# Kernel tuning notes

Measured on AMD Instinct MI355X. Metric: run time of the kernel, lower is better.

The kernel has to match this reference:

```python
import jax, jax.numpy as jnp
import numpy as np

WS = (17, 5, 1)
NT = 23  # 17+5+1 tokens across levels
TABLE_ROWS = (2 * WS[0] - 1) * (2 * WS[0] - 1)  # 1089


def _rel_index():
    cs = []
    for i, w in enumerate(WS):
        c = np.arange(w, dtype=np.float32) - w // 2
        if i < len(WS) - 1:
            c = c * WS[0] / w  # rescale coarser levels to finest grid
        cs.append(c)
    c = np.concatenate(cs)  # [23]
    return (c[:, None] - c[None, :]) + (WS[0] - 1)  # [23,23] float

REL_IDX = jnp.asarray(_rel_index())


def _avgpool1d(x):
    # AvgPool1d(kernel=2, stride=2, padding=1, count_include_pad=False) on last axis (odd L)
    return jnp.concatenate([x[..., :1], (x[..., 1::2] + x[..., 2::2]) * 0.5], axis=-1)


def _l2norm(x):
    n = jnp.linalg.norm(x, axis=-1, keepdims=True)
    return x / jnp.maximum(n, 1e-12)


def _pos_embed(table, abs_bias):
    # table [1089,H], abs_bias [3,H,1,1,1] -> [1,H,1,23,23]
    idx = REL_IDX.reshape(-1)
    fl = jnp.clip(jnp.floor(idx), 0, TABLE_ROWS - 1).astype(jnp.int32)
    ce = jnp.clip(jnp.ceil(idx), 0, TABLE_ROWS - 1).astype(jnp.int32)
    w_ce = (idx - fl.astype(idx.dtype))[:, None]
    pe = (1.0 - w_ce) * table[fl] + w_ce * table[ce]  # [529,H]
    H = table.shape[1]
    pe = pe.reshape(1, 1, NT, NT, H).transpose(0, 4, 1, 2, 3)  # [1,H,1,23,23]
    chunks = jnp.split(pe, [WS[0], WS[0] + WS[1]], axis=3)
    chunks = [c + abs_bias[i][None] for i, c in enumerate(chunks)]
    return jnp.concatenate(chunks, axis=-2)


def _hifi(xh0, xh1, xh2, h_table, h_abs, h_proj_w, h_proj_b):
    q = jnp.concatenate([xh0[0], xh1[0], xh2[0]], axis=-2)  # [B,Hh,hd,23,S]
    k = jnp.concatenate([xh0[1], xh1[1], xh2[1]], axis=-2)
    v = jnp.concatenate([xh0[2], xh1[2], xh2[2]], axis=-2)
    attn = jnp.einsum('bhdts,bhdus->bhdtu', _l2norm(q), _l2norm(k))
    attn = attn + _pos_embed(h_table, h_abs)
    attn = jax.nn.softmax(attn, axis=-1)
    out = jnp.einsum('bhdtu,bhdus->bhdts', attn, v)
    return out @ h_proj_w.T + h_proj_b


def _lofi(xl0, xl1, xl2, l_table, l_abs, l_proj_w, l_proj_b):
    q = jnp.concatenate([xl0[0], xl1[0], xl2[0]], axis=-2)  # [B,Hl,hd,23,S]
    kvs = []
    for i, x in enumerate((xl0, xl1, xl2)):
        kv = x[1:]  # [2,B,Hl,hd,t_i,S]
        if i != 2:  # pool token axis for the two finer levels
            kv = jnp.moveaxis(_avgpool1d(jnp.moveaxis(kv, -2, -1)), -1, -2)
        kvs.append(kv)
    kv = jnp.concatenate(kvs, axis=-2)  # [2,B,Hl,hd,13,S]
    k, v = kv[0], kv[1]
    attn = jnp.einsum('bhdts,bhdus->bhdtu', _l2norm(q), _l2norm(k))  # [B,Hl,hd,23,13]
    pe = _pos_embed(l_table, l_abs)  # [1,Hl,1,23,23]
    Hl = l_table.shape[1]
    p1 = _avgpool1d(pe[..., :WS[0]].reshape(Hl, NT, WS[0])).reshape(1, Hl, 1, NT, -1)
    p2 = _avgpool1d(pe[..., WS[0]:WS[0] + WS[1]].reshape(Hl, NT, WS[1])).reshape(1, Hl, 1, NT, -1)
    p3 = pe[..., -1:]
    attn = attn + jnp.concatenate([p1, p2, p3], axis=-1)
    attn = jax.nn.softmax(attn, axis=-1)
    out = jnp.einsum('bhdtu,bhdus->bhdts', attn, v)
    return out @ l_proj_w.T + l_proj_b


def _forward(xh0, xh1, xh2, xl0, xl1, xl2, h_table, h_abs, l_table, l_abs,
             h_proj_w, h_proj_b, l_proj_w, l_proj_b):
    h_out = _hifi(xh0, xh1, xh2, h_table, h_abs, h_proj_w, h_proj_b)  # [B,1,64,23,S]
    l_out = _lofi(xl0, xl1, xl2, l_table, l_abs, l_proj_w, l_proj_b)  # [B,3,64,23,S]
    return jnp.concatenate([h_out, l_out], axis=1)  # [B,4,64,23,S]


def setup_inputs() -> dict:
    key = jax.random.key(0)
    ks = jax.random.split(key, 14)
    B, hd, S = 4, 64, 1024
    Hh, Hl = 1, 3
    d = {
        'xh0': jax.random.normal(ks[0], (3, B, Hh, hd, 17, S), jnp.float32),
        'xh1': jax.random.normal(ks[1], (3, B, Hh, hd, 5, S), jnp.float32),
        'xh2': jax.random.normal(ks[2], (3, B, Hh, hd, 1, S), jnp.float32),
        'xl0': jax.random.normal(ks[3], (3, B, Hl, hd, 17, S), jnp.float32),
        'xl1': jax.random.normal(ks[4], (3, B, Hl, hd, 5, S), jnp.float32),
        'xl2': jax.random.normal(ks[5], (3, B, Hl, hd, 1, S), jnp.float32),
        'h_table': jax.random.normal(ks[6], (TABLE_ROWS, Hh), jnp.float32) * 0.02,
        'h_abs': jax.random.normal(ks[7], (3, Hh, 1, 1, 1), jnp.float32) * 0.02,
        'l_table': jax.random.normal(ks[8], (TABLE_ROWS, Hl), jnp.float32) * 0.02,
        'l_abs': jax.random.normal(ks[9], (3, Hl, 1, 1, 1), jnp.float32) * 0.02,
        'h_proj_w': jax.random.normal(ks[10], (S, S), jnp.float32) / np.sqrt(S),
        'h_proj_b': jax.random.normal(ks[11], (S,), jnp.float32) * 0.01,
        'l_proj_w': jax.random.normal(ks[12], (S, S), jnp.float32) / np.sqrt(S),
        'l_proj_b': jax.random.normal(ks[13], (S,), jnp.float32) * 0.01,
    }
    return d


def reference(xh0, xh1, xh2, xl0, xl1, xl2, h_table, h_abs, l_table, l_abs,
              h_proj_w, h_proj_b, l_proj_w, l_proj_b):
    return _forward(xh0, xh1, xh2, xl0, xl1, xl2, h_table, h_abs, l_table, l_abs,
                    h_proj_w, h_proj_b, l_proj_w, l_proj_b)
```

## Files before the change

kernel.cpp:

```cpp
#include <hip/hip_runtime.h>
#include <hip/hip_bf16.h>
#include <stdint.h>

#define DEV __device__ __forceinline__

typedef float f32x4 __attribute__((ext_vector_type(4)));
typedef __bf16 bf16x8 __attribute__((ext_vector_type(8)));

DEV __bf16 tobf(float x){
  union { __hip_bfloat16 s; __bf16 b; } u; u.s = __float2bfloat16(x); return u.b;
}
DEV float bflo(uint32_t u){ return __uint_as_float(u << 16); }
DEV float bfhi(uint32_t u){ return __uint_as_float(u & 0xffff0000u); }
DEV float dot4(const float4& a, const float4& b){
  return a.x*b.x + a.y*b.y + a.z*b.z + a.w*b.w;
}
DEV bf16x8 pack8(const float4& a, const float4& b){
  bf16x8 r;
  r[0]=tobf(a.x); r[1]=tobf(a.y); r[2]=tobf(a.z); r[3]=tobf(a.w);
  r[4]=tobf(b.x); r[5]=tobf(b.y); r[6]=tobf(b.z); r[7]=tobf(b.w);
  return r;
}
DEV uint32_t f2bf2(float x, float y){
  union { __hip_bfloat16 b[2]; uint32_t u; } cv;
  cv.b[0] = __float2bfloat16(x); cv.b[1] = __float2bfloat16(y);
  return cv.u;
}
DEV float4 avg4(const float4& a, const float4& b){
  float4 r; r.x=0.5f*(a.x+b.x); r.y=0.5f*(a.y+b.y); r.z=0.5f*(a.z+b.z); r.w=0.5f*(a.w+b.w);
  return r;
}

DEV float relc(int j){
  if (j < 17) return (float)(j - 8);
  if (j < 22) return (float)(j - 19) * 3.4f;
  return 0.0f;
}
DEV int band_of(int t){ return t < 17 ? 0 : (t < 22 ? 1 : 2); }

template<int MODE> DEV void pool_map(int u, int& a, int& b){
  if (MODE == 0){ a = u; b = u; return; }
  if (u == 0){ a = 0; b = 0; }
  else if (u < 9){ a = 2*u - 1; b = 2*u; }
  else if (u == 9){ a = 17; b = 17; }
  else if (u < 12){ a = 2*u - 2; b = 2*u - 1; }
  else { a = 22; b = 22; }
}

DEV float interp_tab(const float* tab, int H, int h, int t, int u){
  float idx = relc(t) - relc(u) + 16.0f;
  float fl = floorf(idx);
  float ce = ceilf(idx);
  int fi = (int)fminf(fmaxf(fl, 0.f), 1088.f);
  int ci = (int)fminf(fmaxf(ce, 0.f), 1088.f);
  float w = idx - fl;
  return (1.0f - w) * tab[fi*H + h] + w * tab[ci*H + h];
}

template<int MODE>
DEV void qk_group(int gm, int qt,
    const float* __restrict__ x0, const float* __restrict__ x1, const float* __restrict__ x2,
    float* __restrict__ SpB,
    float* Spart , float* qnp , float* knp )
{
  constexpr int U = (MODE == 0) ? 23 : 13;
  constexpr int H = (MODE == 0) ? 1 : 3;
  int b, h, d;
  if (MODE == 0){ b = gm >> 6; h = 0; d = gm & 63; }
  else { b = gm / 192; int r = gm % 192; h = r >> 6; d = r & 63; }

  const int tid  = threadIdx.x;
  const int lane = tid & 63;
  const int w    = tid >> 6;
  const int lrow = lane & 15;
  const int kq   = lane >> 4;

  auto base_of = [&](int sel, int band) -> const float* {
    if (band == 0) return x0 + (size_t)((((sel*4 + b)*H + h)*64 + d)*17) * 1024;
    if (band == 1) return x1 + (size_t)((((sel*4 + b)*H + h)*64 + d)*5) * 1024;
    return x2 + (size_t)(((sel*4 + b)*H + h)*64 + d) * 1024;
  };
  const float* qb0 = base_of(0,0); const float* qb1 = base_of(0,1); const float* qb2 = base_of(0,2);
  const float* kb0 = base_of(1,0); const float* kb1 = base_of(1,1); const float* kb2 = base_of(1,2);

  auto rowp = [&](const float* r0, const float* r1, const float* r2, int t) -> const float* {
    if (t < 17) return r0 + (size_t)t * 1024;
    if (t < 22) return r1 + (size_t)(t - 17) * 1024;
    return r2;
  };

  const float* qr[2]; bool qv[2];
  #pragma unroll
  for (int mi = 0; mi < 2; ++mi){
    int t = mi*16 + lrow;
    qv[mi] = (t < 23);
    qr[mi] = qv[mi] ? rowp(qb0,qb1,qb2,t) : qb0;
  }
  const float* krA[2]; const float* krB[2]; bool kv[2];
  #pragma unroll
  for (int ni = 0; ni < 2; ++ni){
    int u = ni*16 + lrow;
    kv[ni] = (u < U);
    int au, bu; pool_map<MODE>(kv[ni] ? u : 0, au, bu);
    krA[ni] = rowp(kb0,kb1,kb2,au);
    krB[ni] = rowp(kb0,kb1,kb2,bu);
  }

  const int sbase = qt*256 + w*64 + kq*8;

  float4 qld[2][4];
  float4 kld[2][4];
  #pragma unroll
  for (int mi = 0; mi < 2; ++mi){
    #pragma unroll
    for (int kk = 0; kk < 2; ++kk){
      #pragma unroll
      for (int hf = 0; hf < 2; ++hf){
        qld[mi][kk*2+hf] = qv[mi] ? *(const float4*)(qr[mi] + sbase + kk*32 + hf*4)
                                  : float4{0,0,0,0};
      }
    }
  }
  if (MODE == 0){
    #pragma unroll
    for (int ni = 0; ni < 2; ++ni){
      #pragma unroll
      for (int kk = 0; kk < 2; ++kk){
        #pragma unroll
        for (int hf = 0; hf < 2; ++hf){
          kld[ni][kk*2+hf] = kv[ni] ? *(const float4*)(krA[ni] + sbase + kk*32 + hf*4)
                                    : float4{0,0,0,0};
        }
      }
    }
  } else {
    #pragma unroll
    for (int kk = 0; kk < 2; ++kk){
      #pragma unroll
      for (int hf = 0; hf < 2; ++hf){
        kld[0][kk*2+hf] = kv[0] ? *(const float4*)(krA[0] + sbase + kk*32 + hf*4)
                                : float4{0,0,0,0};
        kld[1][kk*2+hf] = kv[0] ? *(const float4*)(krB[0] + sbase + kk*32 + hf*4)
                                : float4{0,0,0,0};
      }
    }
  }

  f32x4 acc[2][2] = {};
  float qss[2] = {0.f, 0.f}, kss[2] = {0.f, 0.f};
  #pragma unroll
  for (int kk = 0; kk < 2; ++kk){
    bf16x8 qf[2], kf[2];
    #pragma unroll
    for (int mi = 0; mi < 2; ++mi){
      float4 v0 = qld[mi][kk*2], v1 = qld[mi][kk*2+1];
      qss[mi] += dot4(v0,v0) + dot4(v1,v1);
      qf[mi] = pack8(v0, v1);
    }
    if (MODE == 0){
      #pragma unroll
      for (int ni = 0; ni < 2; ++ni){
        float4 v0 = kld[ni][kk*2], v1 = kld[ni][kk*2+1];
        kss[ni] += dot4(v0,v0) + dot4(v1,v1);
        kf[ni] = pack8(v0, v1);
      }
    } else {
      float4 v0 = avg4(kld[0][kk*2], kld[1][kk*2]);
      float4 v1 = avg4(kld[0][kk*2+1], kld[1][kk*2+1]);
      kss[0] += dot4(v0,v0) + dot4(v1,v1);
      kf[0] = pack8(v0, v1);
    }
    #pragma unroll
    for (int mi = 0; mi < 2; ++mi){
      #pragma unroll
      for (int ni = 0; ni < 2; ++ni){
        if (MODE == 0 || ni == 0)
          acc[mi][ni] = __builtin_amdgcn_mfma_f32_16x16x32_bf16(qf[mi], kf[ni], acc[mi][ni], 0, 0, 0);
      }
    }
  }

  #pragma unroll
  for (int i = 0; i < 2; ++i){
    qss[i] += __shfl_xor(qss[i], 16); qss[i] += __shfl_xor(qss[i], 32);
    kss[i] += __shfl_xor(kss[i], 16); kss[i] += __shfl_xor(kss[i], 32);
  }
  if (lane < 16){
    qnp[w*32 + lane]      = qss[0];
    qnp[w*32 + 16 + lane] = qss[1];
    knp[w*32 + lane]      = kss[0];
    knp[w*32 + 16 + lane] = kss[1];
  }
  #pragma unroll
  for (int mi = 0; mi < 2; ++mi)
    #pragma unroll
    for (int ni = 0; ni < 2; ++ni)
      #pragma unroll
      for (int j = 0; j < 4; ++j)
        Spart[w*1056 + (mi*16 + kq*4 + j)*33 + ni*16 + lrow] = acc[mi][ni][j];
  __syncthreads();

  if (tid < 32){
    SpB[1024 + tid] = qnp[tid] + qnp[32+tid] + qnp[64+tid] + qnp[96+tid];
  } else if (tid < 64){
    int c = tid - 32;
    SpB[1056 + c] = knp[c] + knp[32+c] + knp[64+c] + knp[96+c];
  }
  {
    int r  = tid >> 3;
    int c0 = (tid & 7) * 4;
    float4 o;
    o.x = Spart[r*33+c0+0] + Spart[1056+r*33+c0+0] + Spart[2112+r*33+c0+0] + Spart[3168+r*33+c0+0];
    o.y = Spart[r*33+c0+1] + Spart[1056+r*33+c0+1] + Spart[2112+r*33+c0+1] + Spart[3168+r*33+c0+1];
    o.z = Spart[r*33+c0+2] + Spart[1056+r*33+c0+2] + Spart[2112+r*33+c0+2] + Spart[3168+r*33+c0+2];
    o.w = Spart[r*33+c0+3] + Spart[1056+r*33+c0+3] + Spart[2112+r*33+c0+3] + Spart[3168+r*33+c0+3];
    *(float4*)(SpB + r*32 + c0) = o;
  }
}

__global__ __launch_bounds__(256, 4) void fused_a(
    const float* __restrict__ xh0, const float* __restrict__ xh1, const float* __restrict__ xh2,
    const float* __restrict__ xl0, const float* __restrict__ xl1, const float* __restrict__ xl2,
    const float* __restrict__ htab, const float* __restrict__ habs,
    const float* __restrict__ ltab, const float* __restrict__ labs,
    const float* __restrict__ hw, const float* __restrict__ lw,
    float* __restrict__ Sp, __hip_bfloat16* __restrict__ Vb,
    float* __restrict__ pe_h, float* __restrict__ pe_l,
    __hip_bfloat16* __restrict__ whb, __hip_bfloat16* __restrict__ wlb)
{
  __shared__ __align__(16) float Spart[4*32*33];
  __shared__ float qnp[4*32], knp[4*32];
  const int bid = blockIdx.x;
  const int tid = threadIdx.x;

  if (bid < 4096){
    int g = bid >> 2, qt = bid & 3;
    float* SpB = Sp + (size_t)bid * 1088;
    if (g < 256) qk_group<0>(g,       qt, xh0, xh1, xh2, SpB, Spart, qnp, knp);
    else         qk_group<1>(g - 256, qt, xl0, xl1, xl2, SpB, Spart, qnp, knp);
    return;
  }

  if (bid < 6080){
    const int vb_ = bid - 4096;
    auto vsrc = [&](int r, const float*& pa, const float*& pb){
      if (r < 5888){
        int gg = r / 23, u = r - gg*23;
        int b = gg >> 6, d = gg & 63;
        const float* v0 = xh0 + (size_t)(((8 + b)*64 + d)*17) * 1024;
        const float* v1 = xh1 + (size_t)(((8 + b)*64 + d)*5) * 1024;
        const float* v2 = xh2 + (size_t)((8 + b)*64 + d) * 1024;
        pa = (u < 17) ? v0 + (size_t)u*1024 : (u < 22 ? v1 + (size_t)(u-17)*1024 : v2);
        pb = pa;
      } else {
        int rr = r - 5888;
        int gm = rr / 13, u = rr - gm*13;
        int b = gm / 192, rem = gm % 192, h = rem >> 6, d = rem & 63;
        const float* v0 = xl0 + (size_t)((((8 + b)*3 + h)*64 + d)*17) * 1024;
        const float* v1 = xl1 + (size_t)((((8 + b)*3 + h)*64 + d)*5) * 1024;
        const float* v2 = xl2 + (size_t)(((8 + b)*3 + h)*64 + d) * 1024;
        int au, bu; pool_map<1>(u, au, bu);
        pa = (au < 17) ? v0 + (size_t)au*1024 : (au < 22 ? v1 + (size_t)(au-17)*1024 : v2);
        pb = (bu < 17) ? v0 + (size_t)bu*1024 : (bu < 22 ? v1 + (size_t)(bu-17)*1024 : v2);
      }
    };
    const int c0 = tid * 4;
    float4 va[8], vbv[8]; bool two[8];
    #pragma unroll
    for (int i = 0; i < 8; ++i){
      int r = vb_*8 + i;
      const float *pa, *pb; vsrc(r, pa, pb);
      va[i] = *(const float4*)(pa + c0);
      two[i] = (pb != pa);
      vbv[i] = two[i] ? *(const float4*)(pb + c0) : va[i];
    }
    #pragma unroll
    for (int i = 0; i < 8; ++i){
      float4 a = two[i] ? avg4(va[i], vbv[i]) : va[i];
      uint2 o; o.x = f2bf2(a.x, a.y); o.y = f2bf2(a.z, a.w);
      *(uint2*)(Vb + (size_t)(vb_*8 + i)*1024 + c0) = o;
    }
    return;
  }

  const int pb_ = bid - 6080;
  if (pb_ < 1024){
    int i = (pb_*256 + tid)*8;
    const float* src; __hip_bfloat16* dst;
    if (i < 1048576){ src = hw + i; dst = whb + i; }
    else { src = lw + (i - 1048576); dst = wlb + (i - 1048576); }
    float4 x0 = *(const float4*)(src);
    float4 x1 = *(const float4*)(src + 4);
    uint4 o;
    o.x = f2bf2(x0.x, x0.y); o.y = f2bf2(x0.z, x0.w);
    o.z = f2bf2(x1.x, x1.y); o.w = f2bf2(x1.z, x1.w);
    *(uint4*)dst = o;
  } else if (pb_ == 1024){
    for (int j = tid; j < 529; j += 256){
      int t = j / 23, u = j % 23;
      pe_h[j] = interp_tab(htab, 1, 0, t, u) + habs[band_of(t)];
    }
  } else {
    for (int j = tid; j < 897; j += 256){
      int h = j / 299, r = j % 299, t = r / 13, u = r % 13;
      int a, b; pool_map<1>(u, a, b);
      pe_l[j] = 0.5f * (interp_tab(ltab, 3, h, t, a) + interp_tab(ltab, 3, h, t, b))
              + labs[band_of(t)*3 + h];
    }
  }
}

__global__ __launch_bounds__(256) void gemm_vw(
    const __hip_bfloat16* __restrict__ A,
    const __hip_bfloat16* __restrict__ Wh, const __hip_bfloat16* __restrict__ Wl,
    __hip_bfloat16* __restrict__ VW)
{
  __shared__ __hip_bfloat16 lA[2][128*64];
  __shared__ __hip_bfloat16 lB[2][128*64];
  const int tid  = threadIdx.x;
  const int lane = tid & 63;

  const int bid = blockIdx.x;
  const int swz = (bid & 7) * 124 + (bid >> 3);
  const int mt = swz >> 3, nt = swz & 7;
  const int tM = mt * 128, tN = nt * 128;
  const bool hifi = (mt < 46);
  const __hip_bfloat16* W = hifi ? Wh : Wl;

  const int wm = ((tid >> 6) >> 1) * 64, wn = ((tid >> 6) & 1) * 64;
  f32x4 acc[4][4] = {};

  const int srow = tid >> 3;
  const int scol = ((tid & 7) * 8) ^ ((srow & 7) * 8);
  const __hip_bfloat16* ga = A + (size_t)(tM + srow) * 1024 + scol;
  const __hip_bfloat16* gb = W + (size_t)(tN + srow) * 1024 + scol;

  auto stage = [&](int buf, int k0){
    #pragma unroll
    for (int q = 0; q < 4; ++q){
      __builtin_amdgcn_global_load_lds(
        (const __attribute__((address_space(1))) void*)(ga + k0 + (size_t)q*32*1024),
        (__attribute__((address_space(3))) void*)(&lA[buf][q*2048 + tid*8]), 16, 0, 0);
      __builtin_amdgcn_global_load_lds(
        (const __attribute__((address_space(1))) void*)(gb + k0 + (size_t)q*32*1024),
        (__attribute__((address_space(3))) void*)(&lB[buf][q*2048 + tid*8]), 16, 0, 0);
    }
  };

  const int rsw = (lane & 7) * 8;
  auto compute = [&](int buf){
    #pragma unroll
    for (int kk = 0; kk < 2; ++kk){
      const int cb = (kk*32 + (lane >> 4)*8) ^ rsw;
      bf16x8 af[4], bfr[4];
      #pragma unroll
      for (int mi = 0; mi < 4; ++mi)
        af[mi] = *(const bf16x8*)(&lA[buf][(wm + mi*16 + (lane & 15))*64 + cb]);
      #pragma unroll
      for (int ni = 0; ni < 4; ++ni)
        bfr[ni] = *(const bf16x8*)(&lB[buf][(wn + ni*16 + (lane & 15))*64 + cb]);
      #pragma unroll
      for (int mi = 0; mi < 4; ++mi){
        #pragma unroll
        for (int ni = 0; ni < 4; ++ni)
          acc[mi][ni] = __builtin_amdgcn_mfma_f32_16x16x32_bf16(af[mi], bfr[ni], acc[mi][ni], 0, 0, 0);
      }
    }
  };

  stage(0, 0);
  __syncthreads();
  int cur = 0;
  #pragma unroll 1
  for (int t = 0; t < 15; ++t){
    stage(cur ^ 1, (t + 1) * 64);
    compute(cur);
    __syncthreads();
    cur ^= 1;
  }
  compute(cur);

  #pragma unroll
  for (int mi = 0; mi < 4; ++mi){
    #pragma unroll
    for (int j = 0; j < 4; ++j){
      int r = tM + wm + mi*16 + (lane >> 4)*4 + j;
      __hip_bfloat16* po = VW + (size_t)r * 1024 + tN + wn + (lane & 15);
      #pragma unroll
      for (int ni = 0; ni < 4; ++ni)
        po[ni*16] = __float2bfloat16(acc[mi][ni][j]);
    }
  }
}

template<int MODE>
DEV void mix_group(int g, int sh, int tid,
    const float* __restrict__ Sp, const float* __restrict__ pe,
    const __hip_bfloat16* __restrict__ VW, const float* __restrict__ bias,
    float* __restrict__ out, float* lds_p)
{
  constexpr int U  = (MODE == 0) ? 23 : 13;
  constexpr int UP = (MODE == 0) ? 24 : 16;
  int gm = (MODE == 0) ? g : g - 256;
  int b, h, d;
  if (MODE == 0){ b = gm >> 6; h = 0; d = gm & 63; }
  else { b = gm / 192; int rem = gm % 192; h = rem >> 6; d = rem & 63; }

  {
    int r = tid >> 3, c0 = (tid & 7) * 4;
    const float* A0 = Sp + (size_t)(4*g) * 1088;
    const float* A1 = A0 + 1088;
    const float* A2 = A0 + 2176;
    const float* A3 = A0 + 3264;
    float qn = A0[1024 + r] + A1[1024 + r] + A2[1024 + r] + A3[1024 + r];
    float iqn = 1.0f / fmaxf(sqrtf(qn), 1e-12f);
    float vals[4];
    #pragma unroll
    for (int j = 0; j < 4; ++j){
      int c = c0 + j;
      bool valid = (r < 23) && (c < U);
      if (valid){
        float sv = A0[r*32 + c] + A1[r*32 + c] + A2[r*32 + c] + A3[r*32 + c];
        float kn = A0[1056 + c] + A1[1056 + c] + A2[1056 + c] + A3[1056 + c];
        float ikn = 1.0f / fmaxf(sqrtf(kn), 1e-12f);
        float pv = (MODE == 0) ? pe[r*23 + c] : pe[(h*23 + r)*13 + c];
        vals[j] = sv * iqn * ikn + pv;
      } else vals[j] = -3.0e38f;
    }
    float m = fmaxf(fmaxf(vals[0], vals[1]), fmaxf(vals[2], vals[3]));
    m = fmaxf(m, __shfl_xor(m, 1)); m = fmaxf(m, __shfl_xor(m, 2)); m = fmaxf(m, __shfl_xor(m, 4));
    float e[4], ssum = 0.f;
    #pragma unroll
    for (int j = 0; j < 4; ++j){ e[j] = __expf(vals[j] - m); ssum += e[j]; }
    ssum += __shfl_xor(ssum, 1); ssum += __shfl_xor(ssum, 2); ssum += __shfl_xor(ssum, 4);
    float inv = 1.0f / ssum;
    if (r < 23){
      #pragma unroll
      for (int j = 0; j < 4; ++j)
        lds_p[r*32 + c0 + j] = (c0 + j < U) ? e[j] * inv : 0.f;
    }
  }
  __syncthreads();

  const int s0 = sh*512 + tid*2;
  const uint16_t* vwb = (const uint16_t*)VW +
      ((MODE == 0) ? (size_t)g*23*1024 : (size_t)(5888 + gm*13)*1024) + s0;
  float2 vv[UP];
  #pragma unroll
  for (int u = 0; u < UP; ++u){
    if (u < U){
      uint32_t w2 = *(const uint32_t*)(vwb + (size_t)u*1024);
      vv[u].x = bflo(w2); vv[u].y = bfhi(w2);
    } else { vv[u].x = 0.f; vv[u].y = 0.f; }
  }
  const float bx = bias[s0], by = bias[s0 + 1];
  const int orow0 = (MODE == 0) ? (b*5888 + d*23) : (b*5888 + (1 + h)*1472 + d*23);

  #pragma unroll 2
  for (int t = 0; t < 23; ++t){
    float ax = bx, ay = by;
    #pragma unroll
    for (int u4 = 0; u4 < UP/4; ++u4){
      float4 p = *(const float4*)(lds_p + t*32 + u4*4);
      ax += p.x*vv[u4*4+0].x + p.y*vv[u4*4+1].x + p.z*vv[u4*4+2].x + p.w*vv[u4*4+3].x;
      ay += p.x*vv[u4*4+0].y + p.y*vv[u4*4+1].y + p.z*vv[u4*4+2].y + p.w*vv[u4*4+3].y;
    }
    float2 o2; o2.x = ax; o2.y = ay;
    *(float2*)(out + (size_t)(orow0 + t)*1024 + s0) = o2;
  }
}

__global__ __launch_bounds__(256) void mix_all(
    const float* __restrict__ Sp, const float* __restrict__ pe_h, const float* __restrict__ pe_l,
    const __hip_bfloat16* __restrict__ VW,
    const float* __restrict__ hb, const float* __restrict__ lb,
    float* __restrict__ out)
{
  __shared__ __align__(16) float lds_p[23*32];
  int bid = blockIdx.x;
  int g = bid >> 1, sh = bid & 1;
  if (g < 256) mix_group<0>(g, sh, threadIdx.x, Sp, pe_h, VW, hb, out, lds_p);
  else         mix_group<1>(g, sh, threadIdx.x, Sp, pe_l, VW, lb, out, lds_p);
}

extern "C" void kernel_launch(void* const* d_in, const int* in_sizes, int n_in,
                              void* d_out, int out_size, void* d_ws, size_t ws_size,
                              hipStream_t stream) {
  const float* xh0  = (const float*)d_in[0];
  const float* xh1  = (const float*)d_in[1];
  const float* xh2  = (const float*)d_in[2];
  const float* xl0  = (const float*)d_in[3];
  const float* xl1  = (const float*)d_in[4];
  const float* xl2  = (const float*)d_in[5];
  const float* htab = (const float*)d_in[6];
  const float* habs = (const float*)d_in[7];
  const float* ltab = (const float*)d_in[8];
  const float* labs = (const float*)d_in[9];
  const float* hw   = (const float*)d_in[10];
  const float* hb   = (const float*)d_in[11];
  const float* lw   = (const float*)d_in[12];
  const float* lb   = (const float*)d_in[13];
  float* out = (float*)d_out;

  char* ws = (char*)d_ws;
  float* pe_h = (float*)ws;
  float* pe_l = (float*)(ws + 2176);
  __hip_bfloat16* VW  = (__hip_bfloat16*)(ws + 8192);
  float* Sp           = (float*)(ws + 8192 + 32505856);

  __hip_bfloat16* Vb  = (__hip_bfloat16*)out;
  __hip_bfloat16* whb = (__hip_bfloat16*)(out + 23068672);
  __hip_bfloat16* wlb = whb + 1048576;

  fused_a<<<7106, 256, 0, stream>>>(xh0, xh1, xh2, xl0, xl1, xl2,
                                    htab, habs, ltab, labs, hw, lw,
                                    Sp, Vb, pe_h, pe_l, whb, wlb);
  gemm_vw<<<992, 256, 0, stream>>>(Vb, whb, wlb, VW);
  mix_all<<<2048, 256, 0, stream>>>(Sp, pe_h, pe_l, VW, hb, lb, out);
}
```

Measured before the change: 155.3 us.

## Co-schedule QK score blocks with V·W GEMM blocks in one interleaved launch

Moves the QK score computation out of the first kernel and into a new kernel that interleaves it with the GEMM tiles, one GEMM block for every four QK blocks. The first kernel now only does the V conversion, weight conversion and positional-embedding setup. The aim is to overlap the memory-bound QK work with the MFMA-bound GEMM so both share the GPU at once. In exchange, every block of the combined kernel reserves 64KB of shared memory and launch bounds drop to 2 blocks per SM, which can reduce occupancy for the QK blocks.

```diff
diff --git a/kernel.cpp b/kernel.cpp
--- a/kernel.cpp
+++ b/kernel.cpp
@@ -218,31 +218,100 @@
   }
 }
 
-__global__ __launch_bounds__(256, 4) void fused_a(
+DEV void gemm_block(int gidx, int tid,
+    const __hip_bfloat16* __restrict__ A,
+    const __hip_bfloat16* __restrict__ Wh, const __hip_bfloat16* __restrict__ Wl,
+    __hip_bfloat16* __restrict__ VW,
+    __hip_bfloat16* lA , __hip_bfloat16* lB )
+{
+  const int lane = tid & 63;
+  const int swz = (gidx & 7) * 124 + (gidx >> 3);
+  const int mt = swz >> 3, nt = swz & 7;
+  const int tM = mt * 128, tN = nt * 128;
+  const bool hifi = (mt < 46);
+  const __hip_bfloat16* W = hifi ? Wh : Wl;
+
+  const int wm = ((tid >> 6) >> 1) * 64, wn = ((tid >> 6) & 1) * 64;
+  f32x4 acc[4][4] = {};
+
+  const int srow = tid >> 3;
+  const int scol = ((tid & 7) * 8) ^ ((srow & 7) * 8);
+  const __hip_bfloat16* ga = A + (size_t)(tM + srow) * 1024 + scol;
+  const __hip_bfloat16* gb = W + (size_t)(tN + srow) * 1024 + scol;
+
+  auto stage = [&](int buf, int k0){
+    #pragma unroll
+    for (int q = 0; q < 4; ++q){
+      __builtin_amdgcn_global_load_lds(
+        (const __attribute__((address_space(1))) void*)(ga + k0 + (size_t)q*32*1024),
+        (__attribute__((address_space(3))) void*)(&lA[buf*8192 + q*2048 + tid*8]), 16, 0, 0);
+      __builtin_amdgcn_global_load_lds(
+        (const __attribute__((address_space(1))) void*)(gb + k0 + (size_t)q*32*1024),
+        (__attribute__((address_space(3))) void*)(&lB[buf*8192 + q*2048 + tid*8]), 16, 0, 0);
+    }
+  };
+
+  const int rsw = (lane & 7) * 8;
+  auto compute = [&](int buf){
+    #pragma unroll
+    for (int kk = 0; kk < 2; ++kk){
+      const int cb = (kk*32 + (lane >> 4)*8) ^ rsw;
+      bf16x8 af[4], bfr[4];
+      #pragma unroll
+      for (int mi = 0; mi < 4; ++mi)
+        af[mi] = *(const bf16x8*)(&lA[buf*8192 + (wm + mi*16 + (lane & 15))*64 + cb]);
+      #pragma unroll
+      for (int ni = 0; ni < 4; ++ni)
+        bfr[ni] = *(const bf16x8*)(&lB[buf*8192 + (wn + ni*16 + (lane & 15))*64 + cb]);
+      #pragma unroll
+      for (int mi = 0; mi < 4; ++mi){
+        #pragma unroll
+        for (int ni = 0; ni < 4; ++ni)
+          acc[mi][ni] = __builtin_amdgcn_mfma_f32_16x16x32_bf16(af[mi], bfr[ni], acc[mi][ni], 0, 0, 0);
+      }
+    }
+  };
+
+  stage(0, 0);
+  __syncthreads();
+  int cur = 0;
+  #pragma unroll 1
+  for (int t = 0; t < 15; ++t){
+    stage(cur ^ 1, (t + 1) * 64);
+    compute(cur);
+    __syncthreads();
+    cur ^= 1;
+  }
+  compute(cur);
+
+  #pragma unroll
+  for (int mi = 0; mi < 4; ++mi){
+    #pragma unroll
+    for (int j = 0; j < 4; ++j){
+      int r = tM + wm + mi*16 + (lane >> 4)*4 + j;
+      __hip_bfloat16* po = VW + (size_t)r * 1024 + tN + wn + (lane & 15);
+      #pragma unroll
+      for (int ni = 0; ni < 4; ++ni)
+        po[ni*16] = __float2bfloat16(acc[mi][ni][j]);
+    }
+  }
+}
+
+__global__ __launch_bounds__(256, 4) void fused_vp(
     const float* __restrict__ xh0, const float* __restrict__ xh1, const float* __restrict__ xh2,
     const float* __restrict__ xl0, const float* __restrict__ xl1, const float* __restrict__ xl2,
     const float* __restrict__ htab, const float* __restrict__ habs,
     const float* __restrict__ ltab, const float* __restrict__ labs,
     const float* __restrict__ hw, const float* __restrict__ lw,
-    float* __restrict__ Sp, __hip_bfloat16* __restrict__ Vb,
+    __hip_bfloat16* __restrict__ Vb,
     float* __restrict__ pe_h, float* __restrict__ pe_l,
     __hip_bfloat16* __restrict__ whb, __hip_bfloat16* __restrict__ wlb)
 {
-  __shared__ __align__(16) float Spart[4*32*33];
-  __shared__ float qnp[4*32], knp[4*32];
   const int bid = blockIdx.x;
   const int tid = threadIdx.x;
 
-  if (bid < 4096){
-    int g = bid >> 2, qt = bid & 3;
-    float* SpB = Sp + (size_t)bid * 1088;
-    if (g < 256) qk_group<0>(g,       qt, xh0, xh1, xh2, SpB, Spart, qnp, knp);
-    else         qk_group<1>(g - 256, qt, xl0, xl1, xl2, SpB, Spart, qnp, knp);
-    return;
-  }
-
-  if (bid < 6080){
-    const int vb_ = bid - 4096;
+  if (bid < 1984){
+    const int vb_ = bid;
     auto vsrc = [&](int r, const float*& pa, const float*& pb){
       if (r < 5888){
         int gg = r / 23, u = r - gg*23;
@@ -283,7 +352,7 @@
     return;
   }
 
-  const int pb_ = bid - 6080;
+  const int pb_ = bid - 1984;
   if (pb_ < 1024){
     int i = (pb_*256 + tid)*8;
     const float* src; __hip_bfloat16* dst;
@@ -310,87 +379,35 @@
   }
 }
 
-__global__ __launch_bounds__(256) void gemm_vw(
-    const __hip_bfloat16* __restrict__ A,
-    const __hip_bfloat16* __restrict__ Wh, const __hip_bfloat16* __restrict__ Wl,
+__global__ __launch_bounds__(256, 2) void fused_qg(
+    const float* __restrict__ xh0, const float* __restrict__ xh1, const float* __restrict__ xh2,
+    const float* __restrict__ xl0, const float* __restrict__ xl1, const float* __restrict__ xl2,
+    float* __restrict__ Sp,
+    const __hip_bfloat16* __restrict__ Vb,
+    const __hip_bfloat16* __restrict__ whb, const __hip_bfloat16* __restrict__ wlb,
     __hip_bfloat16* __restrict__ VW)
 {
-  __shared__ __hip_bfloat16 lA[2][128*64];
-  __shared__ __hip_bfloat16 lB[2][128*64];
-  const int tid  = threadIdx.x;
-  const int lane = tid & 63;
-
+  __shared__ __align__(16) char smem[65536];
   const int bid = blockIdx.x;
-  const int swz = (bid & 7) * 124 + (bid >> 3);
-  const int mt = swz >> 3, nt = swz & 7;
-  const int tM = mt * 128, tN = nt * 128;
-  const bool hifi = (mt < 46);
-  const __hip_bfloat16* W = hifi ? Wh : Wl;
-
-  const int wm = ((tid >> 6) >> 1) * 64, wn = ((tid >> 6) & 1) * 64;
-  f32x4 acc[4][4] = {};
-
-  const int srow = tid >> 3;
-  const int scol = ((tid & 7) * 8) ^ ((srow & 7) * 8);
-  const __hip_bfloat16* ga = A + (size_t)(tM + srow) * 1024 + scol;
-  const __hip_bfloat16* gb = W + (size_t)(tN + srow) * 1024 + scol;
-
-  auto stage = [&](int buf, int k0){
-    #pragma unroll
-    for (int q = 0; q < 4; ++q){
-      __builtin_amdgcn_global_load_lds(
-        (const __attribute__((address_space(1))) void*)(ga + k0 + (size_t)q*32*1024),
-        (__attribute__((address_space(3))) void*)(&lA[buf][q*2048 + tid*8]), 16, 0, 0);
-      __builtin_amdgcn_global_load_lds(
-        (const __attribute__((address_space(1))) void*)(gb + k0 + (size_t)q*32*1024),
-        (__attribute__((address_space(3))) void*)(&lB[buf][q*2048 + tid*8]), 16, 0, 0);
-    }
-  };
-
-  const int rsw = (lane & 7) * 8;
-  auto compute = [&](int buf){
-    #pragma unroll
-    for (int kk = 0; kk < 2; ++kk){
-      const int cb = (kk*32 + (lane >> 4)*8) ^ rsw;
-      bf16x8 af[4], bfr[4];
-      #pragma unroll
-      for (int mi = 0; mi < 4; ++mi)
-        af[mi] = *(const bf16x8*)(&lA[buf][(wm + mi*16 + (lane & 15))*64 + cb]);
-      #pragma unroll
-      for (int ni = 0; ni < 4; ++ni)
-        bfr[ni] = *(const bf16x8*)(&lB[buf][(wn + ni*16 + (lane & 15))*64 + cb]);
-      #pragma unroll
-      for (int mi = 0; mi < 4; ++mi){
-        #pragma unroll
-        for (int ni = 0; ni < 4; ++ni)
-          acc[mi][ni] = __builtin_amdgcn_mfma_f32_16x16x32_bf16(af[mi], bfr[ni], acc[mi][ni], 0, 0, 0);
-      }
-    }
-  };
-
-  stage(0, 0);
-  __syncthreads();
-  int cur = 0;
-  #pragma unroll 1
-  for (int t = 0; t < 15; ++t){
-    stage(cur ^ 1, (t + 1) * 64);
-    compute(cur);
-    __syncthreads();
-    cur ^= 1;
-  }
-  compute(cur);
-
-  #pragma unroll
-  for (int mi = 0; mi < 4; ++mi){
-    #pragma unroll
-    for (int j = 0; j < 4; ++j){
-      int r = tM + wm + mi*16 + (lane >> 4)*4 + j;
-      __hip_bfloat16* po = VW + (size_t)r * 1024 + tN + wn + (lane & 15);
-      #pragma unroll
-      for (int ni = 0; ni < 4; ++ni)
-        po[ni*16] = __float2bfloat16(acc[mi][ni][j]);
-    }
-  }
+  const int tid = threadIdx.x;
+
+  if ((bid % 5) == 4){
+    int gidx = bid / 5;
+    if (gidx < 992){
+      gemm_block(gidx, tid, Vb, whb, wlb, VW,
+                 (__hip_bfloat16*)smem, (__hip_bfloat16*)(smem + 32768));
+    }
+    return;
+  }
+
+  int qidx = (bid / 5) * 4 + (bid % 5);
+  float* Spart = (float*)smem;
+  float* qnp   = Spart + 4224;
+  float* knp   = qnp + 128;
+  int g = qidx >> 2, qt = qidx & 3;
+  float* SpB = Sp + (size_t)qidx * 1088;
+  if (g < 256) qk_group<0>(g,       qt, xh0, xh1, xh2, SpB, Spart, qnp, knp);
+  else         qk_group<1>(g - 256, qt, xl0, xl1, xl2, SpB, Spart, qnp, knp);
 }
 
 template<int MODE>
@@ -512,9 +529,10 @@
   __hip_bfloat16* whb = (__hip_bfloat16*)(out + 23068672);
   __hip_bfloat16* wlb = whb + 1048576;
 
-  fused_a<<<7106, 256, 0, stream>>>(xh0, xh1, xh2, xl0, xl1, xl2,
-                                    htab, habs, ltab, labs, hw, lw,
-                                    Sp, Vb, pe_h, pe_l, whb, wlb);
-  gemm_vw<<<992, 256, 0, stream>>>(Vb, whb, wlb, VW);
+  fused_vp<<<3010, 256, 0, stream>>>(xh0, xh1, xh2, xl0, xl1, xl2,
+                                     htab, habs, ltab, labs, hw, lw,
+                                     Vb, pe_h, pe_l, whb, wlb);
+  fused_qg<<<5120, 256, 0, stream>>>(xh0, xh1, xh2, xl0, xl1, xl2,
+                                     Sp, Vb, whb, wlb, VW);
   mix_all<<<2048, 256, 0, stream>>>(Sp, pe_h, pe_l, VW, hb, lb, out);
 }
```

After: 159.3 us. 1.03x slower.
